# Kernel tuning notes

Hardware: AMD Instinct MI355X
Metric: run time of the kernel (lower is better)

The kernel has to match this reference:

```python
import jax, jax.numpy as jnp
import numpy as np

# TT-factorized linear: 784 = 7*4*7*4 -> 512 = 4*4*8*4, max_rank=20
# canonical TT ranks: [1, 20, 20, 16, 1] (r3 capped by m4*n4 = 16)
B = 16384
R1, R2, R3 = 20, 20, 16


def setup_inputs() -> dict:
    key = jax.random.key(0)
    k = jax.random.split(key, 6)
    x = jax.random.normal(k[0], (B, 784), jnp.float32)
    # TT cores G_k[r_{k-1}, m_k, n_k, r_k] with boundary ranks squeezed
    core1 = jax.random.normal(k[1], (7, 4, R1), jnp.float32) * 0.3   # [m1,n1,r1]
    core2 = jax.random.normal(k[2], (R1, 4, 4, R2), jnp.float32) * 0.1  # [r1,m2,n2,r2]
    core3 = jax.random.normal(k[3], (R2, 7, 8, R3), jnp.float32) * 0.05  # [r2,m3,n3,r3]
    core4 = jax.random.normal(k[4], (R3, 4, 4), jnp.float32) * 0.1   # [r3,m4,n4]
    bias = jax.random.normal(k[5], (512,), jnp.float32) * 0.01
    return {"x": x, "core1": core1, "core2": core2, "core3": core3,
            "core4": core4, "bias": bias}


def reference(x, core1, core2, core3, core4, bias):
    b = x.shape[0]
    # reshape input into TT mode factorization [B, m1, m2, m3, m4]
    x5 = x.reshape(b, 7, 4, 7, 4)
    # chain of small core contractions (the fusion-opportunity op pattern)
    t = jnp.einsum('bijkl,ipr->bjklpr', x5, core1)   # [B,4,7,4, n1,r1]
    t = jnp.einsum('bjklpr,rjqs->bklpqs', t, core2)  # [B,7,4, n1,n2,r2]
    t = jnp.einsum('bklpqs,sket->blpqet', t, core3)  # [B,4, n1,n2,n3,r3]
    y = jnp.einsum('blpqet,tlf->bpqef', t, core4)    # [B, n1,n2,n3,n4]
    y = y.reshape(b, 512) + bias
    # original forward: relu then softmax over features.
    # NOTE: the source calls self.fc2(y) but discards the result, so it is
    # omitted here (no effect on output).
    return jax.nn.softmax(jax.nn.relu(y), axis=1)
```

## Files before the change

kernel.cpp:

```cpp
#include <hip/hip_runtime.h>


typedef __attribute__((ext_vector_type(8))) short short8;
typedef __attribute__((ext_vector_type(4))) float floatx4;

__device__ __forceinline__ unsigned int pack2_bf16(float a, float b) {
    unsigned int ua = __float_as_uint(a);
    unsigned int ub = __float_as_uint(b);
    return ((ub + 0x8000u) & 0xFFFF0000u) | ((ua + 0x8000u) >> 16);
}

__device__ __forceinline__ short f32_to_bf16_rne(float v) {
    unsigned int u = __float_as_uint(v);
    return (short)(((u + 0x7FFFu + ((u >> 16) & 1)) >> 16) & 0xFFFF);
}

__global__ void prep_all(const float* __restrict__ c1, const float* __restrict__ c2,
                         const float* __restrict__ c3, const float* __restrict__ c4,
                         short* __restrict__ wp) {
    const int tid = threadIdx.x;
    const int blk = blockIdx.x;
    if (blk == 28) {
        for (int e = tid; e < 8192; e += 256) {
            int j   = e & 7;
            int lid = (e >> 3) & 15;
            int q2  = (e >> 7) & 1;
            int tn  = e >> 8;
            wp[(((tn * 25 + 24) * 64 + (2 + q2) * 16 + lid) << 3) + j] = 0;
        }
        return;
    }
    __shared__ float t12s[320];
    __shared__ float t123s[7 * 2048];
    __shared__ float c4s[256];
    const int ij = blk;
    const int i = ij >> 2, j2 = ij & 3;

    if (tid < 256) c4s[tid] = c4[tid];
    for (int e = tid; e < 320; e += 256) {
        int s = e % 20, pq = e / 20;
        int p = pq >> 2, q = pq & 3;
        float acc = 0.f;
        #pragma unroll
        for (int r = 0; r < 20; ++r)
            acc += c1[i * 80 + p * 20 + r] * c2[r * 320 + j2 * 80 + q * 20 + s];
        t12s[e] = acc;
    }
    __syncthreads();

    for (int e = tid; e < 14336; e += 256) {
        int k3 = e >> 11, li = e & 2047;
        int t = li & 15, pqe = li >> 4;
        int e3 = pqe & 7, pq = pqe >> 3;
        float acc = 0.f;
        const float* tp = t12s + pq * 20;
        const float* cp = c3 + k3 * 128 + e3 * 16 + t;
        #pragma unroll
        for (int s = 0; s < 20; ++s) acc += tp[s] * cp[s * 896];
        t123s[e] = acc;
    }
    __syncthreads();

    for (int e = tid; e < 28 * 512; e += 256) {
        int kl = e >> 9, n = e & 511;
        int k  = ij * 28 + kl;
        int k3 = kl >> 2, l = kl & 3;
        int f4 = n & 3, e3 = (n >> 2) & 7, q = (n >> 5) & 3, p = n >> 7;
        int pqe = p * 32 + q * 8 + e3;
        const float* tp = t123s + k3 * 2048 + pqe * 16;
        const float* cq = c4s + l * 4 + f4;
        float a = 0.f;
        #pragma unroll
        for (int t = 0; t < 16; ++t) a += tp[t] * cq[t * 16];
        int tk = k >> 5, quad = (k >> 3) & 3, j = k & 7;
        int tn = n >> 4, lid = n & 15;
        wp[(((tn * 25 + tk) * 64 + quad * 16 + lid) << 3) + j] = f32_to_bf16_rne(a);
    }
}

__global__ __launch_bounds__(512, 4) void tt_gemm(const float* __restrict__ x,
                                                  const short* __restrict__ wp,
                                                  const float* __restrict__ bias,
                                                  float* __restrict__ out) {
    __shared__ __align__(16) short s_a[3200 * 8];
    __shared__ float part[8][32];

    const int tid  = threadIdx.x;
    const int w    = tid >> 6;
    const int lane = tid & 63;
    const int quad = lane >> 4;
    const int lid  = lane & 15;
    const int m_base = blockIdx.x * 32;

    for (int a = tid; a < 3200; a += 512) {
        const int row = ((a >> 6) & 1) * 16 + (a & 15);
        const int kch = (a >> 7) * 4 + ((a >> 4) & 3);
        const int kc  = kch * 8;
        floatx4 v0 = {0.f, 0.f, 0.f, 0.f}, v1 = {0.f, 0.f, 0.f, 0.f};
        if (kc < 784) {
            const floatx4* p = (const floatx4*)(x + (size_t)(m_base + row) * 784 + kc);
            v0 = p[0]; v1 = p[1];
        }
        union { short8 s; unsigned int u[4]; } af;
        af.u[0] = pack2_bf16(v0.x, v0.y);
        af.u[1] = pack2_bf16(v0.z, v0.w);
        af.u[2] = pack2_bf16(v1.x, v1.y);
        af.u[3] = pack2_bf16(v1.z, v1.w);
        *(short8*)&s_a[a * 8] = af.s;
    }
    __syncthreads();

    const short* sa  = s_a + lane * 8;
    const short* wpw = wp + ((size_t)(w * 4) * 25 * 64 + lane) * 8;

    floatx4 acc[2][4];
    #pragma unroll
    for (int mt = 0; mt < 2; ++mt)
        #pragma unroll
        for (int nt = 0; nt < 4; ++nt)
            acc[mt][nt] = floatx4{0.f, 0.f, 0.f, 0.f};

    short8 a_f[2][2], b_f[2][4];
    a_f[0][0] = *(const short8*)(sa);
    a_f[0][1] = *(const short8*)(sa + 64 * 8);
    #pragma unroll
    for (int nt = 0; nt < 4; ++nt)
        b_f[0][nt] = *(const short8*)(wpw + (size_t)(nt * 25) * 64 * 8);

    #pragma unroll
    for (int tk = 0; tk < 25; ++tk) {
        const int cur = tk & 1, nxt = cur ^ 1;
        if (tk < 24) {
            const short* sa2 = sa + (size_t)(tk + 1) * 128 * 8;
            a_f[nxt][0] = *(const short8*)(sa2);
            a_f[nxt][1] = *(const short8*)(sa2 + 64 * 8);
            #pragma unroll
            for (int nt = 0; nt < 4; ++nt)
                b_f[nxt][nt] = *(const short8*)(wpw + (size_t)(nt * 25 + tk + 1) * 64 * 8);
        }
        #pragma unroll
        for (int nt = 0; nt < 4; ++nt) {
            acc[0][nt] = __builtin_amdgcn_mfma_f32_16x16x32_bf16(a_f[cur][0], b_f[cur][nt], acc[0][nt], 0, 0, 0);
            acc[1][nt] = __builtin_amdgcn_mfma_f32_16x16x32_bf16(a_f[cur][1], b_f[cur][nt], acc[1][nt], 0, 0, 0);
        }
    }

    float bias_v[4];
    #pragma unroll
    for (int nt = 0; nt < 4; ++nt)
        bias_v[nt] = bias[w * 64 + nt * 16 + lid];

    #pragma unroll
    for (int mt = 0; mt < 2; ++mt) {
        #pragma unroll
        for (int reg = 0; reg < 4; ++reg) {
            float s = 0.f;
            #pragma unroll
            for (int nt = 0; nt < 4; ++nt) {
                float v = acc[mt][nt][reg] + bias_v[nt];
                v = fmaxf(v, 0.f);
                float e = __expf(v);
                acc[mt][nt][reg] = e;
                s += e;
            }
            s += __shfl_xor(s, 1, 64);
            s += __shfl_xor(s, 2, 64);
            s += __shfl_xor(s, 4, 64);
            s += __shfl_xor(s, 8, 64);
            if (lid == 0) part[w][mt * 16 + quad * 4 + reg] = s;
        }
    }
    __syncthreads();

    #pragma unroll
    for (int mt = 0; mt < 2; ++mt) {
        #pragma unroll
        for (int reg = 0; reg < 4; ++reg) {
            const int row = mt * 16 + quad * 4 + reg;
            float tot = 0.f;
            #pragma unroll
            for (int ww = 0; ww < 8; ++ww) tot += part[ww][row];
            const float inv = 1.0f / tot;
            #pragma unroll
            for (int nt = 0; nt < 4; ++nt)
                out[(size_t)(m_base + row) * 512 + w * 64 + nt * 16 + lid] = acc[mt][nt][reg] * inv;
        }
    }
}

extern "C" void kernel_launch(void* const* d_in, const int* in_sizes, int n_in,
                              void* d_out, int out_size, void* d_ws, size_t ws_size,
                              hipStream_t stream) {
    const float* x    = (const float*)d_in[0];
    const float* c1   = (const float*)d_in[1];
    const float* c2   = (const float*)d_in[2];
    const float* c3   = (const float*)d_in[3];
    const float* c4   = (const float*)d_in[4];
    const float* bias = (const float*)d_in[5];
    float* out = (float*)d_out;
    short* wpb = (short*)d_ws;

    prep_all<<<29,  256, 0, stream>>>(c1, c2, c3, c4, wpb);
    tt_gemm <<<512, 512, 0, stream>>>(x, wpb, bias, out);
}
```

Measured before the change: 148.5 us.

## Split weight-prep across 225 blocks and deepen B-fragment prefetch

The TT-core contraction kernel is split so each of the 28 (i,j2) tiles is processed by 8 blocks, one per 64-column output strip, cutting per-block work and shared memory and raising parallelism from 29 to 225 blocks. The GEMM kernel now prefetches weight fragments two K-steps ahead with a triple buffer, and issues the first two loads before the x staging loop so global weight latency overlaps the A-tile conversion. Each prep block recomputes the small t12 product redundantly, and the extra register buffers raise register pressure under the 512x4 launch bound.

```diff
diff --git a/kernel.cpp b/kernel.cpp
--- a/kernel.cpp
+++ b/kernel.cpp
@@ -20,7 +20,7 @@
                          short* __restrict__ wp) {
     const int tid = threadIdx.x;
     const int blk = blockIdx.x;
-    if (blk == 28) {
+    if (blk == 224) {
         for (int e = tid; e < 8192; e += 256) {
             int j   = e & 7;
             int lid = (e >> 3) & 15;
@@ -31,29 +31,34 @@
         return;
     }
     __shared__ float t12s[320];
-    __shared__ float t123s[7 * 2048];
+    __shared__ float t123s[7 * 256];
     __shared__ float c4s[256];
-    const int ij = blk;
-    const int i = ij >> 2, j2 = ij & 3;
+
+    const int ij    = blk >> 3;
+    const int strip = blk & 7;
+    const int i  = ij >> 2, j2 = ij & 3;
+    const int p  = strip >> 1;
+    const int qh = strip & 1;
 
     if (tid < 256) c4s[tid] = c4[tid];
     for (int e = tid; e < 320; e += 256) {
         int s = e % 20, pq = e / 20;
-        int p = pq >> 2, q = pq & 3;
+        int pp = pq >> 2, q = pq & 3;
         float acc = 0.f;
         #pragma unroll
         for (int r = 0; r < 20; ++r)
-            acc += c1[i * 80 + p * 20 + r] * c2[r * 320 + j2 * 80 + q * 20 + s];
+            acc += c1[i * 80 + pp * 20 + r] * c2[r * 320 + j2 * 80 + q * 20 + s];
         t12s[e] = acc;
     }
     __syncthreads();
 
-    for (int e = tid; e < 14336; e += 256) {
-        int k3 = e >> 11, li = e & 2047;
-        int t = li & 15, pqe = li >> 4;
-        int e3 = pqe & 7, pq = pqe >> 3;
+    for (int e = tid; e < 1792; e += 256) {
+        int k3 = e >> 8, li = e & 255;
+        int t = li & 15, pql = li >> 4;
+        int qloc = pql >> 3, e3 = pql & 7;
+        int q = 2 * qh + qloc;
         float acc = 0.f;
-        const float* tp = t12s + pq * 20;
+        const float* tp = t12s + (p * 4 + q) * 20;
         const float* cp = c3 + k3 * 128 + e3 * 16 + t;
         #pragma unroll
         for (int s = 0; s < 20; ++s) acc += tp[s] * cp[s * 896];
@@ -61,13 +66,14 @@
     }
     __syncthreads();
 
-    for (int e = tid; e < 28 * 512; e += 256) {
-        int kl = e >> 9, n = e & 511;
-        int k  = ij * 28 + kl;
+    for (int e = tid; e < 1792; e += 256) {
+        int kl = e >> 6, nl = e & 63;
+        int k = ij * 28 + kl;
+        int n = strip * 64 + nl;
         int k3 = kl >> 2, l = kl & 3;
-        int f4 = n & 3, e3 = (n >> 2) & 7, q = (n >> 5) & 3, p = n >> 7;
-        int pqe = p * 32 + q * 8 + e3;
-        const float* tp = t123s + k3 * 2048 + pqe * 16;
+        int f4 = n & 3, e3 = (n >> 2) & 7;
+        int pql = ((n >> 5) & 1) * 8 + e3;
+        const float* tp = t123s + k3 * 256 + pql * 16;
         const float* cq = c4s + l * 4 + f4;
         float a = 0.f;
         #pragma unroll
@@ -92,14 +98,22 @@
     const int lid  = lane & 15;
     const int m_base = blockIdx.x * 32;
 
+    const short* wpw = wp + ((size_t)(w * 4) * 25 * 64 + lane) * 8;
+
+    short8 b_f[3][4];
+    #pragma unroll
+    for (int nt = 0; nt < 4; ++nt) {
+        b_f[0][nt] = *(const short8*)(wpw + (size_t)(nt * 25 + 0) * 64 * 8);
+        b_f[1][nt] = *(const short8*)(wpw + (size_t)(nt * 25 + 1) * 64 * 8);
+    }
+
     for (int a = tid; a < 3200; a += 512) {
         const int row = ((a >> 6) & 1) * 16 + (a & 15);
-        const int kch = (a >> 7) * 4 + ((a >> 4) & 3);
-        const int kc  = kch * 8;
+        const int kc  = ((a >> 7) * 4 + ((a >> 4) & 3)) * 8;
         floatx4 v0 = {0.f, 0.f, 0.f, 0.f}, v1 = {0.f, 0.f, 0.f, 0.f};
         if (kc < 784) {
-            const floatx4* p = (const floatx4*)(x + (size_t)(m_base + row) * 784 + kc);
-            v0 = p[0]; v1 = p[1];
+            const floatx4* pp = (const floatx4*)(x + (size_t)(m_base + row) * 784 + kc);
+            v0 = pp[0]; v1 = pp[1];
         }
         union { short8 s; unsigned int u[4]; } af;
         af.u[0] = pack2_bf16(v0.x, v0.y);
@@ -110,8 +124,7 @@
     }
     __syncthreads();
 
-    const short* sa  = s_a + lane * 8;
-    const short* wpw = wp + ((size_t)(w * 4) * 25 * 64 + lane) * 8;
+    const short* sa = s_a + lane * 8;
 
     floatx4 acc[2][4];
     #pragma unroll
@@ -120,28 +133,26 @@
         for (int nt = 0; nt < 4; ++nt)
             acc[mt][nt] = floatx4{0.f, 0.f, 0.f, 0.f};
 
-    short8 a_f[2][2], b_f[2][4];
+    short8 a_f[2][2];
     a_f[0][0] = *(const short8*)(sa);
     a_f[0][1] = *(const short8*)(sa + 64 * 8);
-    #pragma unroll
-    for (int nt = 0; nt < 4; ++nt)
-        b_f[0][nt] = *(const short8*)(wpw + (size_t)(nt * 25) * 64 * 8);
 
     #pragma unroll
     for (int tk = 0; tk < 25; ++tk) {
-        const int cur = tk & 1, nxt = cur ^ 1;
-        if (tk < 24) {
+        if (tk + 2 < 25) {
+            #pragma unroll
+            for (int nt = 0; nt < 4; ++nt)
+                b_f[(tk + 2) % 3][nt] = *(const short8*)(wpw + (size_t)(nt * 25 + tk + 2) * 64 * 8);
+        }
+        if (tk + 1 < 25) {
             const short* sa2 = sa + (size_t)(tk + 1) * 128 * 8;
-            a_f[nxt][0] = *(const short8*)(sa2);
-            a_f[nxt][1] = *(const short8*)(sa2 + 64 * 8);
-            #pragma unroll
-            for (int nt = 0; nt < 4; ++nt)
-                b_f[nxt][nt] = *(const short8*)(wpw + (size_t)(nt * 25 + tk + 1) * 64 * 8);
+            a_f[(tk + 1) & 1][0] = *(const short8*)(sa2);
+            a_f[(tk + 1) & 1][1] = *(const short8*)(sa2 + 64 * 8);
         }
         #pragma unroll
         for (int nt = 0; nt < 4; ++nt) {
-            acc[0][nt] = __builtin_amdgcn_mfma_f32_16x16x32_bf16(a_f[cur][0], b_f[cur][nt], acc[0][nt], 0, 0, 0);
-            acc[1][nt] = __builtin_amdgcn_mfma_f32_16x16x32_bf16(a_f[cur][1], b_f[cur][nt], acc[1][nt], 0, 0, 0);
+            acc[0][nt] = __builtin_amdgcn_mfma_f32_16x16x32_bf16(a_f[tk & 1][0], b_f[tk % 3][nt], acc[0][nt], 0, 0, 0);
+            acc[1][nt] = __builtin_amdgcn_mfma_f32_16x16x32_bf16(a_f[tk & 1][1], b_f[tk % 3][nt], acc[1][nt], 0, 0, 0);
         }
     }
 
@@ -200,6 +211,6 @@
     float* out = (float*)d_out;
     short* wpb = (short*)d_ws;
 
-    prep_all<<<29,  256, 0, stream>>>(c1, c2, c3, c4, wpb);
+    prep_all<<<225, 256, 0, stream>>>(c1, c2, c3, c4, wpb);
     tt_gemm <<<512, 512, 0, stream>>>(x, wpb, bias, out);
 }
```

Measured after the change: 125.7 us. 1.18x faster.
